# Optimization experiments

Hardware: AMD Instinct MI355X
Metric: run time of the kernel (lower is better)

The kernel has to match this reference:

```python
import jax, jax.numpy as jnp
import numpy as np

N, D, R, E, H = 100000, 128, 4, 150000, 8
DK = D // H  # 16


def setup_inputs() -> dict:
    key = jax.random.key(0)
    ks = jax.random.split(key, 12)
    w_scale = 1.0 / np.sqrt(D)
    rel_scale = 1.0 / np.sqrt(DK)
    return {
        'x': jax.random.normal(ks[0], (N, D), dtype=jnp.float32),
        'edges_src': jax.random.randint(ks[1], (R, E), 0, N, dtype=jnp.int32),
        'edges_dst': jax.random.randint(ks[2], (R, E), 0, N, dtype=jnp.int32),
        'Wk': jax.random.normal(ks[3], (D, D), dtype=jnp.float32) * w_scale,
        'bk': jnp.zeros((D,), dtype=jnp.float32),
        'Wq': jax.random.normal(ks[4], (D, D), dtype=jnp.float32) * w_scale,
        'bq': jnp.zeros((D,), dtype=jnp.float32),
        'Wv': jax.random.normal(ks[5], (D, D), dtype=jnp.float32) * w_scale,
        'bv': jnp.zeros((D,), dtype=jnp.float32),
        'Wa': jax.random.normal(ks[6], (D, D), dtype=jnp.float32) * w_scale,
        'ba': jnp.zeros((D,), dtype=jnp.float32),
        'rel_att': jax.random.normal(ks[7], (R, H, DK, DK), dtype=jnp.float32) * rel_scale,
        'rel_msg': jax.random.normal(ks[8], (R, H, DK, DK), dtype=jnp.float32) * rel_scale,
        'rel_pri': jnp.ones((R, H), dtype=jnp.float32),
        'skip': jnp.ones((1,), dtype=jnp.float32),
    }


def reference(x, edges_src, edges_dst, Wk, bk, Wq, bq, Wv, bv, Wa, ba,
              rel_att, rel_msg, rel_pri, skip):
    n, d = x.shape
    r, e = edges_src.shape
    h, dk = rel_att.shape[1], rel_att.shape[2]
    sqrt_dk = jnp.sqrt(jnp.asarray(dk, dtype=x.dtype))

    # per-type k/q/v projections (single node type) -> [N, H, dk]
    k = (x @ Wk.T + bk).reshape(n, h, dk)
    q = (x @ Wq.T + bq).reshape(n, h, dk)
    v = (x @ Wv.T + bv).reshape(n, h, dk)

    # edge_attention: per-relation per-head dk x dk transforms on gathered src feats
    key_e = jnp.einsum('rehd,rhdf->rehf', k[edges_src], rel_att)   # [R,E,H,dk]
    att = (q[edges_dst] * key_e).sum(-1) * rel_pri[:, None, :] / sqrt_dk  # [R,E,H]
    val = jnp.einsum('rehd,rhdf->rehf', v[edges_src], rel_msg)     # [R,E,H,dk]

    # mailbox softmax per (relation, dst node, head) via segment ops
    seg = (edges_dst.astype(jnp.int32) + jnp.arange(r, dtype=jnp.int32)[:, None] * n).reshape(-1)
    att_f = att.reshape(r * e, h)
    m = jax.ops.segment_max(att_f, seg, num_segments=r * n)
    a = jnp.exp(att_f - m[seg])
    s = jax.ops.segment_sum(a, seg, num_segments=r * n)
    attn = a / s[seg]                                              # [R*E, H]

    # softmax-weighted scatter aggregation -> [R, N, H*dk]
    msg = (attn[:, :, None] * val.reshape(r * e, h, dk)).reshape(r * e, h * dk)
    t = jax.ops.segment_sum(msg, seg, num_segments=r * n).reshape(r, n, d)
    t = t.mean(axis=0)  # cross_reducer='mean' over relations

    # skip-gated output linear (dropout is identity in eval)
    alpha = jax.nn.sigmoid(skip[0])
    return (t @ Wa.T + ba) * alpha + x * (1.0 - alpha)
```

## Files before the change

### kernel.cpp

```cpp
#include <hip/hip_runtime.h>

#define NN 100000
#define DD 128
#define RR 4
#define EE 150000
#define HH 8
#define DK 16

#define NSEG (RR * NN)
#define NEDGE (RR * EE)
#define SCAN_BLK 256
#define SCAN_ELEMS 1024
#define SCAN_NB ((NSEG + SCAN_ELEMS - 1) / SCAN_ELEMS)
#define PAD_K 136
#define MAT_U 132
#define ND2 (NN * 64)
#define WMAT 8192

typedef short bf16x8 __attribute__((ext_vector_type(8)));
typedef float f32x4  __attribute__((ext_vector_type(4)));

__device__ __forceinline__ unsigned short f2bf(float f) {
    unsigned u = __float_as_uint(f);
    return (unsigned short)((u + 0x7fffu + ((u >> 16) & 1u)) >> 16);
}
__device__ __forceinline__ float bflo(unsigned w) { return __uint_as_float(w << 16); }
__device__ __forceinline__ float bfhi(unsigned w) { return __uint_as_float(w & 0xffff0000u); }

__device__ __forceinline__ int wswz(int n, int c) {
    int ks = c >> 4, kg = (c >> 2) & 3, e = c & 3;
    int wc = n >> 6, j = (n >> 4) & 3, lrow = n & 15;
    return ((((ks * 2 + wc) * 4 + j) * 64) + kg * 16 + lrow) * 4 + e;
}

__global__ __launch_bounds__(256) void prep_pack(
    const float* __restrict__ Wk, const float* __restrict__ bk,
    const float* __restrict__ Wq, const float* __restrict__ bq,
    unsigned* __restrict__ wAll, float* __restrict__ bAll)
{
    const int b = blockIdx.x;
    const float* W = b ? Wq : Wk;
    const float* bias = b ? bq : bk;
    unsigned* out = wAll + b * WMAT;
    const int tid = threadIdx.x;
    #pragma unroll
    for (int i = 0; i < 32; ++i) {
        int idx = tid + 256 * i;
        float2 v = *(const float2*)(W + idx * 2);
        unsigned u = (unsigned)f2bf(v.x) | ((unsigned)f2bf(v.y) << 16);
        out[wswz(idx >> 6, idx & 63)] = u;
    }
    if (tid < 128) bAll[b * 128 + tid] = bias[tid];
}

__global__ __launch_bounds__(128) void prep_wmsg(
    const float* __restrict__ Wv, const float* __restrict__ bv,
    const float* __restrict__ rel_msg,
    unsigned* __restrict__ wAll, float* __restrict__ bAll)
{
    const int b = blockIdx.x;
    const int r = b >> 3, h = b & 7;
    const int c = threadIdx.x;
    __shared__ float Msh[256];
    __shared__ float sh2[16][128];
    for (int i = c; i < 256; i += 128) Msh[i] = rel_msg[(b << 8) + i];
    __syncthreads();

    #pragma unroll 4
    for (int f = 0; f < 16; ++f) {
        float acc = 0.f;
        #pragma unroll
        for (int d = 0; d < 16; ++d)
            acc = __builtin_fmaf(Msh[d * 16 + f], Wv[(h * 16 + d) * DD + c], acc);
        sh2[f][c] = acc;
    }
    if (c < 16) {
        float acc = 0.f;
        #pragma unroll
        for (int d = 0; d < 16; ++d)
            acc = __builtin_fmaf(Msh[d * 16 + c], bv[h * 16 + d], acc);
        bAll[(2 + r) * 128 + h * 16 + c] = acc;
    }
    __syncthreads();

    unsigned* out = wAll + (2 + r) * WMAT;
    #pragma unroll
    for (int k = 0; k < 8; ++k) {
        int idx = c * 8 + k;
        int f = idx >> 6, jc = idx & 63;
        unsigned u = (unsigned)f2bf(sh2[f][2 * jc]) | ((unsigned)f2bf(sh2[f][2 * jc + 1]) << 16);
        out[wswz(h * 16 + f, jc)] = u;
    }
}

__global__ __launch_bounds__(256) void mfma_proj(
    const float* __restrict__ X,
    const unsigned* __restrict__ wAll, const float* __restrict__ bAll,
    unsigned* __restrict__ kb, unsigned* __restrict__ qb, unsigned* __restrict__ vMb)
{
    const int tid = threadIdx.x;
    const int lane = tid & 63;
    const int wave = tid >> 6;
    const int wr = wave >> 1;
    const int wc = wave & 1;
    const long m0 = (long)blockIdx.x * 64;
    const int mp = blockIdx.y * 2;

    __shared__ short Xs[64 * PAD_K];

    #pragma unroll
    for (int i = 0; i < 8; ++i) {
        int f = tid + 256 * i;
        int row = f >> 5, c4 = f & 31;
        long m = m0 + row;
        float4 v = make_float4(0.f, 0.f, 0.f, 0.f);
        if (m < NN) v = ((const float4*)(X + m * DD))[c4];
        unsigned u0 = (unsigned)f2bf(v.x) | ((unsigned)f2bf(v.y) << 16);
        unsigned u1 = (unsigned)f2bf(v.z) | ((unsigned)f2bf(v.w) << 16);
        *(uint2*)&Xs[row * PAD_K + c4 * 4] = make_uint2(u0, u1);
    }
    __syncthreads();

    const int lrow = lane & 15;
    const int kg = lane >> 4;

    #pragma unroll
    for (int mm = 0; mm < 2; ++mm) {
        const int mat = mp + mm;
        const unsigned* Wp = wAll + mat * WMAT;
        const float* bias = bAll + mat * 128;
        unsigned* outb = (mat == 0) ? kb : (mat == 1) ? qb : (vMb + (long)(mat - 2) * ND2);

        f32x4 acc[2][4];
        #pragma unroll
        for (int i = 0; i < 2; ++i)
            #pragma unroll
            for (int j = 0; j < 4; ++j) acc[i][j] = (f32x4){0.f, 0.f, 0.f, 0.f};

        #pragma unroll
        for (int ks = 0; ks < 4; ++ks) {
            const int kk = ks * 32 + kg * 8;
            bf16x8 xf[2], wf[4];
            #pragma unroll
            for (int i = 0; i < 2; ++i)
                xf[i] = *(const bf16x8*)&Xs[(wr * 32 + i * 16 + lrow) * PAD_K + kk];
            #pragma unroll
            for (int j = 0; j < 4; ++j)
                wf[j] = *(const bf16x8*)(Wp + (((ks * 2 + wc) * 4 + j) << 8) + (lane << 2));
            #pragma unroll
            for (int i = 0; i < 2; ++i)
                #pragma unroll
                for (int j = 0; j < 4; ++j)
                    acc[i][j] = __builtin_amdgcn_mfma_f32_16x16x32_bf16(wf[j], xf[i], acc[i][j], 0, 0, 0);
        }

        #pragma unroll
        for (int j = 0; j < 4; ++j) {
            const int nb = wc * 64 + j * 16 + kg * 4;
            const float b0 = bias[nb + 0], b1 = bias[nb + 1];
            const float b2 = bias[nb + 2], b3 = bias[nb + 3];
            #pragma unroll
            for (int i = 0; i < 2; ++i) {
                long m = m0 + wr * 32 + i * 16 + lrow;
                if (m < NN) {
                    unsigned u0 = (unsigned)f2bf(acc[i][j][0] + b0) | ((unsigned)f2bf(acc[i][j][1] + b1) << 16);
                    unsigned u1 = (unsigned)f2bf(acc[i][j][2] + b2) | ((unsigned)f2bf(acc[i][j][3] + b3) << 16);
                    *(uint2*)&outb[m * 64 + (nb >> 1)] = make_uint2(u0, u1);
                }
            }
        }
    }
}

__global__ __launch_bounds__(256) void mfma_out(
    const unsigned* __restrict__ Tp, const float* __restrict__ Wa, const float* __restrict__ ba,
    float* __restrict__ out, const float* __restrict__ skip, const float* __restrict__ xres)
{
    const int tid = threadIdx.x;
    const int lane = tid & 63;
    const int wave = tid >> 6;
    const int wr = wave >> 1;
    const int wc = wave & 1;
    const long m0 = (long)blockIdx.x * 64;

    __shared__ short Xs[64 * PAD_K];
    __shared__ short Wsh[128 * PAD_K];

    #pragma unroll
    for (int i = 0; i < 4; ++i) {
        int f = tid + 256 * i;
        int row = f >> 4, c = f & 15;
        long m = m0 + row;
        uint4 v = make_uint4(0u, 0u, 0u, 0u);
        if (m < NN) v = ((const uint4*)(Tp + m * 64))[c];
        *(uint4*)&Xs[row * PAD_K + c * 8] = v;
    }
    #pragma unroll
    for (int i = 0; i < 16; ++i) {
        int f = tid + 256 * i;
        int row = f >> 5, c4 = f & 31;
        float4 v = ((const float4*)(Wa + row * DD))[c4];
        unsigned u0 = (unsigned)f2bf(v.x) | ((unsigned)f2bf(v.y) << 16);
        unsigned u1 = (unsigned)f2bf(v.z) | ((unsigned)f2bf(v.w) << 16);
        *(uint2*)&Wsh[row * PAD_K + c4 * 4] = make_uint2(u0, u1);
    }
    __syncthreads();

    const int lrow = lane & 15;
    const int kg = lane >> 4;

    f32x4 acc[2][4];
    #pragma unroll
    for (int i = 0; i < 2; ++i)
        #pragma unroll
        for (int j = 0; j < 4; ++j) acc[i][j] = (f32x4){0.f, 0.f, 0.f, 0.f};

    #pragma unroll
    for (int ks = 0; ks < 4; ++ks) {
        const int kk = ks * 32 + kg * 8;
        bf16x8 xf[2], wf[4];
        #pragma unroll
        for (int i = 0; i < 2; ++i)
            xf[i] = *(const bf16x8*)&Xs[(wr * 32 + i * 16 + lrow) * PAD_K + kk];
        #pragma unroll
        for (int j = 0; j < 4; ++j)
            wf[j] = *(const bf16x8*)&Wsh[(wc * 64 + j * 16 + lrow) * PAD_K + kk];
        #pragma unroll
        for (int i = 0; i < 2; ++i)
            #pragma unroll
            for (int j = 0; j < 4; ++j)
                acc[i][j] = __builtin_amdgcn_mfma_f32_16x16x32_bf16(xf[i], wf[j], acc[i][j], 0, 0, 0);
    }

    const float s = 1.f / (1.f + __expf(-skip[0]));
    const float al = s, bt = 1.f - s;

    #pragma unroll
    for (int j = 0; j < 4; ++j) {
        const int n = wc * 64 + j * 16 + lrow;
        const float bcol = ba[n];
        #pragma unroll
        for (int i = 0; i < 2; ++i) {
            #pragma unroll
            for (int r = 0; r < 4; ++r) {
                long m = m0 + wr * 32 + i * 16 + kg * 4 + r;
                if (m < NN) {
                    long o = m * DD + n;
                    out[o] = __builtin_fmaf(xres[o], bt, (acc[i][j][r] + bcol) * al);
                }
            }
        }
    }
}


__global__ __launch_bounds__(256) void csr_hist(
    const int* __restrict__ edst, int* __restrict__ cnt)
{
    int idx = blockIdx.x * 256 + threadIdx.x;
    if (idx >= NEDGE) return;
    int r = idx / EE;
    atomicAdd(&cnt[r * NN + edst[idx]], 1);
}

__global__ __launch_bounds__(SCAN_BLK) void scan1(
    const int* __restrict__ cnt, int* __restrict__ offs, int* __restrict__ bsum)
{
    __shared__ int sh[SCAN_BLK];
    int blk = blockIdx.x, tid = threadIdx.x;
    int base = blk * SCAN_ELEMS + tid * 4;
    int v0 = 0, v1 = 0, v2 = 0, v3 = 0;
    if (base + 3 < NSEG) {
        int4 t = *(const int4*)(cnt + base);
        v0 = t.x; v1 = t.y; v2 = t.z; v3 = t.w;
    } else {
        if (base + 0 < NSEG) v0 = cnt[base + 0];
        if (base + 1 < NSEG) v1 = cnt[base + 1];
        if (base + 2 < NSEG) v2 = cnt[base + 2];
        if (base + 3 < NSEG) v3 = cnt[base + 3];
    }
    int tsum = v0 + v1 + v2 + v3;
    sh[tid] = tsum;
    __syncthreads();
    #pragma unroll
    for (int d = 1; d < SCAN_BLK; d <<= 1) {
        int x = (tid >= d) ? sh[tid - d] : 0;
        __syncthreads();
        sh[tid] += x;
        __syncthreads();
    }
    int excl = sh[tid] - tsum;
    int r0 = excl, r1 = r0 + v0, r2 = r1 + v1, r3 = r2 + v2;
    if (base + 3 < NSEG) {
        *(int4*)(offs + base) = make_int4(r0, r1, r2, r3);
    } else {
        if (base + 0 < NSEG) offs[base + 0] = r0;
        if (base + 1 < NSEG) offs[base + 1] = r1;
        if (base + 2 < NSEG) offs[base + 2] = r2;
        if (base + 3 < NSEG) offs[base + 3] = r3;
    }
    if (tid == SCAN_BLK - 1) bsum[blk] = sh[tid];
}

__global__ __launch_bounds__(512) void scan2(int* __restrict__ bsum)
{
    __shared__ int sh[512];
    int tid = threadIdx.x;
    int v = (tid < SCAN_NB) ? bsum[tid] : 0;
    sh[tid] = v;
    __syncthreads();
    #pragma unroll
    for (int d = 1; d < 512; d <<= 1) {
        int x = (tid >= d) ? sh[tid - d] : 0;
        __syncthreads();
        sh[tid] += x;
        __syncthreads();
    }
    if (tid < SCAN_NB) bsum[tid] = sh[tid] - v;
}

__global__ __launch_bounds__(SCAN_BLK) void scan3(
    int* __restrict__ offs, int* __restrict__ cur, const int* __restrict__ bsum)
{
    int blk = blockIdx.x;
    int add = bsum[blk];
    int base = blk * SCAN_ELEMS + threadIdx.x * 4;
    #pragma unroll
    for (int j = 0; j < 4; ++j)
        if (base + j < NSEG) {
            int v = offs[base + j] + add;
            offs[base + j] = v;
            cur[base + j] = v;
        }
}

__global__ __launch_bounds__(256) void csr_fill(
    const int* __restrict__ esrc, const int* __restrict__ edst,
    int* __restrict__ cur, int* __restrict__ csr_src)
{
    int idx = blockIdx.x * 256 + threadIdx.x;
    if (idx >= NEDGE) return;
    int r = idx / EE;
    int pos = atomicAdd(&cur[r * NN + edst[idx]], 1);
    csr_src[pos] = esrc[idx];
}

#define GT 512
__global__ __launch_bounds__(GT) void gather_agg(
    const unsigned* __restrict__ kb, const unsigned* __restrict__ qbuf,
    const unsigned* __restrict__ vMb,
    const int* __restrict__ csr_src, const int* __restrict__ offs,
    const float* __restrict__ rel_att, const float* __restrict__ rel_pri,
    unsigned* __restrict__ tb)
{
    __shared__ unsigned As[32 * MAT_U];
    __shared__ float prish[32];
    const int tid = threadIdx.x;
    #pragma unroll
    for (int i = 0; i < (32 * 128) / GT; ++i) {
        int f = tid + GT * i;
        int m = f >> 7, j = f & 127;
        float2 a = *(const float2*)(rel_att + m * 256 + j * 2);
        As[m * MAT_U + j] = (unsigned)f2bf(a.x) | ((unsigned)f2bf(a.y) << 16);
    }
    if (tid < 32) prish[tid] = rel_pri[tid] * 0.25f;
    __syncthreads();

    int gidx = blockIdx.x * GT + tid;
    if (gidx >= NN * HH) return;
    const int dst = gidx >> 3, h = gidx & 7;

    float qh[16];
    {
        const uint4* qp = (const uint4*)(qbuf + (long)dst * 64 + h * 8);
        uint4 qa = qp[0], qc = qp[1];
        qh[0] = bflo(qa.x);  qh[1] = bfhi(qa.x);
        qh[2] = bflo(qa.y);  qh[3] = bfhi(qa.y);
        qh[4] = bflo(qa.z);  qh[5] = bfhi(qa.z);
        qh[6] = bflo(qa.w);  qh[7] = bfhi(qa.w);
        qh[8] = bflo(qc.x);  qh[9] = bfhi(qc.x);
        qh[10] = bflo(qc.y); qh[11] = bfhi(qc.y);
        qh[12] = bflo(qc.z); qh[13] = bfhi(qc.z);
        qh[14] = bflo(qc.w); qh[15] = bfhi(qc.w);
    }

    float tacc[16];
    #pragma unroll
    for (int f = 0; f < 16; ++f) tacc[f] = 0.f;

    for (int r = 0; r < RR; ++r) {
        const int seg = r * NN + dst;
        const int beg = offs[seg];
        const int end = (seg == NSEG - 1) ? NEDGE : offs[seg + 1];
        if (end <= beg) continue;

        const unsigned* A = &As[(r * HH + h) * MAT_U];
        const float pri = prish[r * HH + h];

        float qbar[16];
        #pragma unroll
        for (int d = 0; d < 16; ++d) {
            uint4 r0 = *(const uint4*)&A[d * 8];
            uint4 r1 = *(const uint4*)&A[d * 8 + 4];
            float acc = bflo(r0.x) * qh[0];
            acc = __builtin_fmaf(bfhi(r0.x), qh[1], acc);
            acc = __builtin_fmaf(bflo(r0.y), qh[2], acc);
            acc = __builtin_fmaf(bfhi(r0.y), qh[3], acc);
            acc = __builtin_fmaf(bflo(r0.z), qh[4], acc);
            acc = __builtin_fmaf(bfhi(r0.z), qh[5], acc);
            acc = __builtin_fmaf(bflo(r0.w), qh[6], acc);
            acc = __builtin_fmaf(bfhi(r0.w), qh[7], acc);
            acc = __builtin_fmaf(bflo(r1.x), qh[8], acc);
            acc = __builtin_fmaf(bfhi(r1.x), qh[9], acc);
            acc = __builtin_fmaf(bflo(r1.y), qh[10], acc);
            acc = __builtin_fmaf(bfhi(r1.y), qh[11], acc);
            acc = __builtin_fmaf(bflo(r1.z), qh[12], acc);
            acc = __builtin_fmaf(bfhi(r1.z), qh[13], acc);
            acc = __builtin_fmaf(bflo(r1.w), qh[14], acc);
            acc = __builtin_fmaf(bfhi(r1.w), qh[15], acc);
            qbar[d] = acc * pri;
        }

        float s = 0.f;
        float vb[16];
        #pragma unroll
        for (int f = 0; f < 16; ++f) vb[f] = 0.f;

        const unsigned* vMr = vMb + (long)r * ND2;
        for (int e = beg; e < end; ++e) {
            int src = csr_src[e];
            const uint4* kp = (const uint4*)(kb + (long)src * 64 + h * 8);
            uint4 ka = kp[0], kc = kp[1];
            const uint4* vp = (const uint4*)(vMr + (long)src * 64 + h * 8);
            uint4 va = vp[0], vc = vp[1];

            float att;
            att  = bflo(ka.x) * qbar[0];
            att = __builtin_fmaf(bfhi(ka.x), qbar[1], att);
            att = __builtin_fmaf(bflo(ka.y), qbar[2], att);
            att = __builtin_fmaf(bfhi(ka.y), qbar[3], att);
            att = __builtin_fmaf(bflo(ka.z), qbar[4], att);
            att = __builtin_fmaf(bfhi(ka.z), qbar[5], att);
            att = __builtin_fmaf(bflo(ka.w), qbar[6], att);
            att = __builtin_fmaf(bfhi(ka.w), qbar[7], att);
            att = __builtin_fmaf(bflo(kc.x), qbar[8], att);
            att = __builtin_fmaf(bfhi(kc.x), qbar[9], att);
            att = __builtin_fmaf(bflo(kc.y), qbar[10], att);
            att = __builtin_fmaf(bfhi(kc.y), qbar[11], att);
            att = __builtin_fmaf(bflo(kc.z), qbar[12], att);
            att = __builtin_fmaf(bfhi(kc.z), qbar[13], att);
            att = __builtin_fmaf(bflo(kc.w), qbar[14], att);
            att = __builtin_fmaf(bfhi(kc.w), qbar[15], att);

            float ea = __expf(att);
            s += ea;
            vb[0]  = __builtin_fmaf(ea, bflo(va.x), vb[0]);
            vb[1]  = __builtin_fmaf(ea, bfhi(va.x), vb[1]);
            vb[2]  = __builtin_fmaf(ea, bflo(va.y), vb[2]);
            vb[3]  = __builtin_fmaf(ea, bfhi(va.y), vb[3]);
            vb[4]  = __builtin_fmaf(ea, bflo(va.z), vb[4]);
            vb[5]  = __builtin_fmaf(ea, bfhi(va.z), vb[5]);
            vb[6]  = __builtin_fmaf(ea, bflo(va.w), vb[6]);
            vb[7]  = __builtin_fmaf(ea, bfhi(va.w), vb[7]);
            vb[8]  = __builtin_fmaf(ea, bflo(vc.x), vb[8]);
            vb[9]  = __builtin_fmaf(ea, bfhi(vc.x), vb[9]);
            vb[10] = __builtin_fmaf(ea, bflo(vc.y), vb[10]);
            vb[11] = __builtin_fmaf(ea, bfhi(vc.y), vb[11]);
            vb[12] = __builtin_fmaf(ea, bflo(vc.z), vb[12]);
            vb[13] = __builtin_fmaf(ea, bfhi(vc.z), vb[13]);
            vb[14] = __builtin_fmaf(ea, bflo(vc.w), vb[14]);
            vb[15] = __builtin_fmaf(ea, bfhi(vc.w), vb[15]);
        }

        float inv = 1.f / s;
        #pragma unroll
        for (int f = 0; f < 16; ++f)
            tacc[f] = __builtin_fmaf(vb[f], inv, tacc[f]);
    }

    unsigned* tp = tb + (long)dst * 64 + h * 8;
    uint4 o0, o1;
    o0.x = (unsigned)f2bf(tacc[0] * 0.25f)  | ((unsigned)f2bf(tacc[1] * 0.25f) << 16);
    o0.y = (unsigned)f2bf(tacc[2] * 0.25f)  | ((unsigned)f2bf(tacc[3] * 0.25f) << 16);
    o0.z = (unsigned)f2bf(tacc[4] * 0.25f)  | ((unsigned)f2bf(tacc[5] * 0.25f) << 16);
    o0.w = (unsigned)f2bf(tacc[6] * 0.25f)  | ((unsigned)f2bf(tacc[7] * 0.25f) << 16);
    o1.x = (unsigned)f2bf(tacc[8] * 0.25f)  | ((unsigned)f2bf(tacc[9] * 0.25f) << 16);
    o1.y = (unsigned)f2bf(tacc[10] * 0.25f) | ((unsigned)f2bf(tacc[11] * 0.25f) << 16);
    o1.z = (unsigned)f2bf(tacc[12] * 0.25f) | ((unsigned)f2bf(tacc[13] * 0.25f) << 16);
    o1.w = (unsigned)f2bf(tacc[14] * 0.25f) | ((unsigned)f2bf(tacc[15] * 0.25f) << 16);
    ((uint4*)tp)[0] = o0;
    ((uint4*)tp)[1] = o1;
}

extern "C" void kernel_launch(void* const* d_in, const int* in_sizes, int n_in,
                              void* d_out, int out_size, void* d_ws, size_t ws_size,
                              hipStream_t stream)
{
    const float* x   = (const float*)d_in[0];
    const int* esrc  = (const int*)d_in[1];
    const int* edst  = (const int*)d_in[2];
    const float* Wk  = (const float*)d_in[3];
    const float* bk  = (const float*)d_in[4];
    const float* Wq  = (const float*)d_in[5];
    const float* bq  = (const float*)d_in[6];
    const float* Wv  = (const float*)d_in[7];
    const float* bv  = (const float*)d_in[8];
    const float* Wa  = (const float*)d_in[9];
    const float* ba  = (const float*)d_in[10];
    const float* rel_att = (const float*)d_in[11];
    const float* rel_msg = (const float*)d_in[12];
    const float* rel_pri = (const float*)d_in[13];
    const float* skip    = (const float*)d_in[14];
    float* out = (float*)d_out;

    unsigned* wsu = (unsigned*)d_ws;
    unsigned* tbp = wsu;
    unsigned* qb  = tbp + ND2;
    unsigned* kb  = qb + ND2;
    unsigned* vMb = kb + ND2;
    unsigned* wAll = vMb + 4L * ND2;
    float* bAll = (float*)(wAll + 6 * WMAT);
    int* cnt  = (int*)(bAll + 768);
    int* offs = cnt + NSEG;
    int* cur  = offs + NSEG;
    int* bsum = cur + NSEG;
    int* csr  = bsum + 512;

    hipMemsetAsync(cnt, 0, NSEG * sizeof(int), stream);

    prep_pack<<<2, 256, 0, stream>>>(Wk, bk, Wq, bq, wAll, bAll);
    prep_wmsg<<<32, 128, 0, stream>>>(Wv, bv, rel_msg, wAll, bAll);

    const int gb = (NN + 63) / 64;
    mfma_proj<<<dim3(gb, 3), 256, 0, stream>>>(x, wAll, bAll, kb, qb, vMb);

    const int ebk = (NEDGE + 255) / 256;
    csr_hist<<<ebk, 256, 0, stream>>>(edst, cnt);
    scan1<<<SCAN_NB, SCAN_BLK, 0, stream>>>(cnt, offs, bsum);
    scan2<<<1, 512, 0, stream>>>(bsum);
    scan3<<<SCAN_NB, SCAN_BLK, 0, stream>>>(offs, cur, bsum);
    csr_fill<<<ebk, 256, 0, stream>>>(esrc, edst, cur, csr);

    gather_agg<<<(NN * HH + GT - 1) / GT, GT, 0, stream>>>(
        kb, qb, vMb, csr, offs, rel_att, rel_pri, tbp);

    mfma_out<<<gb, 256, 0, stream>>>(tbp, Wa, ba, out, skip, x);
}
```

Measured before the change: 307.7 us.

## Sort destination nodes by in-degree to balance gather_agg workload

```diff
diff --git a/kernel.cpp b/kernel.cpp
--- a/kernel.cpp
+++ b/kernel.cpp
@@ -345,11 +345,56 @@
     csr_src[pos] = esrc[idx];
 }
 
+__global__ __launch_bounds__(256) void deg_hist(
+    const int* __restrict__ offs, int* __restrict__ deg, int* __restrict__ dhist)
+{
+    int i = blockIdx.x * 256 + threadIdx.x;
+    if (i >= NN) return;
+    int d = 0;
+    #pragma unroll
+    for (int r = 0; r < RR; ++r) {
+        int seg = r * NN + i;
+        int beg = offs[seg];
+        int end = (seg == NSEG - 1) ? NEDGE : offs[seg + 1];
+        d += end - beg;
+    }
+    d = min(d, 1023);
+    deg[i] = d;
+    atomicAdd(&dhist[d], 1);
+}
+
+__global__ __launch_bounds__(1024) void deg_scan(
+    const int* __restrict__ dhist, int* __restrict__ dcur)
+{
+    __shared__ int sh[1024];
+    int tid = threadIdx.x;
+    int v = dhist[tid];
+    sh[tid] = v;
+    __syncthreads();
+    for (int d = 1; d < 1024; d <<= 1) {
+        int x = (tid >= d) ? sh[tid - d] : 0;
+        __syncthreads();
+        sh[tid] += x;
+        __syncthreads();
+    }
+    dcur[tid] = sh[tid] - v;
+}
+
+__global__ __launch_bounds__(256) void deg_fill(
+    const int* __restrict__ deg, int* __restrict__ dcur, int* __restrict__ order)
+{
+    int i = blockIdx.x * 256 + threadIdx.x;
+    if (i >= NN) return;
+    int pos = atomicAdd(&dcur[deg[i]], 1);
+    order[pos] = i;
+}
+
 #define GT 512
 __global__ __launch_bounds__(GT) void gather_agg(
     const unsigned* __restrict__ kb, const unsigned* __restrict__ qbuf,
     const unsigned* __restrict__ vMb,
     const int* __restrict__ csr_src, const int* __restrict__ offs,
+    const int* __restrict__ order,
     const float* __restrict__ rel_att, const float* __restrict__ rel_pri,
     unsigned* __restrict__ tb)
 {
@@ -368,7 +413,8 @@
 
     int gidx = blockIdx.x * GT + tid;
     if (gidx >= NN * HH) return;
-    const int dst = gidx >> 3, h = gidx & 7;
+    const int dst = order[gidx >> 3];
+    const int h = gidx & 7;
 
     float qh[16];
     {
@@ -520,13 +566,17 @@
     unsigned* vMb = kb + ND2;
     unsigned* wAll = vMb + 4L * ND2;
     float* bAll = (float*)(wAll + 6 * WMAT);
-    int* cnt  = (int*)(bAll + 768);
-    int* offs = cnt + NSEG;
-    int* cur  = offs + NSEG;
-    int* bsum = cur + NSEG;
-    int* csr  = bsum + 512;
-
-    hipMemsetAsync(cnt, 0, NSEG * sizeof(int), stream);
+    int* cnt   = (int*)(bAll + 768);
+    int* dhist = cnt + NSEG;
+    int* dcur  = dhist + 1024;
+    int* offs  = dcur + 1024;
+    int* cur   = offs + NSEG;
+    int* bsum  = cur + NSEG;
+    int* csr   = bsum + 512;
+    int* deg   = csr + NEDGE;
+    int* order = deg + NN;
+
+    hipMemsetAsync(cnt, 0, (NSEG + 2048) * sizeof(int), stream);
 
     prep_pack<<<2, 256, 0, stream>>>(Wk, bk, Wq, bq, wAll, bAll);
     prep_wmsg<<<32, 128, 0, stream>>>(Wv, bv, rel_msg, wAll, bAll);
@@ -541,8 +591,13 @@
     scan3<<<SCAN_NB, SCAN_BLK, 0, stream>>>(offs, cur, bsum);
     csr_fill<<<ebk, 256, 0, stream>>>(esrc, edst, cur, csr);
 
+    const int nbk = (NN + 255) / 256;
+    deg_hist<<<nbk, 256, 0, stream>>>(offs, deg, dhist);
+    deg_scan<<<1, 1024, 0, stream>>>(dhist, dcur);
+    deg_fill<<<nbk, 256, 0, stream>>>(deg, dcur, order);
+
     gather_agg<<<(NN * HH + GT - 1) / GT, GT, 0, stream>>>(
-        kb, qb, vMb, csr, offs, rel_att, rel_pri, tbp);
+        kb, qb, vMb, csr, offs, order, rel_att, rel_pri, tbp);
 
     mfma_out<<<gb, 256, 0, stream>>>(tbp, Wa, ba, out, skip, x);
 }
```

Result: slower. 1.049 ms (+240.9%).
